# Performance work log

Hardware: AMD Instinct MI355X
Metric: run time of the kernel (lower is better)

The kernel has to match this reference:

```python
import jax, jax.numpy as jnp
import numpy as np

B, L, D, H, DFF = 2, 2048, 1024, 16, 4096
DH = D // H  # 64
EPS = 1e-6


def setup_inputs() -> dict:
    key = jax.random.key(0)
    ks = jax.random.split(key, 12)
    s = 0.02  # weight init scale
    inp = {
        "x": jax.random.normal(ks[0], (B, L, D), jnp.float32),
        "Wq": jax.random.normal(ks[1], (D, D), jnp.float32) * s,
        "bq": jnp.zeros((D,), jnp.float32),
        "Wk": jax.random.normal(ks[2], (D, D), jnp.float32) * s,
        "bk": jnp.zeros((D,), jnp.float32),
        "Wv": jax.random.normal(ks[3], (D, D), jnp.float32) * s,
        "bv": jnp.zeros((D,), jnp.float32),
        "Wo": jax.random.normal(ks[4], (D, D), jnp.float32) * s,
        "bo": jnp.zeros((D,), jnp.float32),
        "E": jax.random.normal(ks[5], (L, DH), jnp.float32),  # max_seq==L rel. embeddings
        "W1": jax.random.normal(ks[6], (D, DFF), jnp.float32) * s,
        "b1": jnp.zeros((DFF,), jnp.float32),
        "W2": jax.random.normal(ks[7], (DFF, D), jnp.float32) * s,
        "b2": jnp.zeros((D,), jnp.float32),
        "g1": jnp.ones((D,), jnp.float32),
        "beta1": jnp.zeros((D,), jnp.float32),
        "g2": jnp.ones((D,), jnp.float32),
        "beta2": jnp.zeros((D,), jnp.float32),
    }
    return inp


def _layernorm(x, g, b):
    mu = jnp.mean(x, axis=-1, keepdims=True)
    var = jnp.mean(jnp.square(x - mu), axis=-1, keepdims=True)
    return (x - mu) * jax.lax.rsqrt(var + EPS) * g + b


def _qe_mask(qe):
    # keep entries where col j >= len_k - 1 - row i (upper-right triangle)
    lq, lk = qe.shape[-2], qe.shape[-1]
    keep = jnp.arange(lk)[None, :] >= (lk - 1 - jnp.arange(lq))[:, None]
    return qe * keep.astype(qe.dtype)


def _skew(qe):
    # Music-Transformer skewing: pad 1 on the left of last dim, reshape, drop first row
    b, h, lq, lk = qe.shape
    padded = jnp.pad(qe, ((0, 0), (0, 0), (0, 0), (1, 0)))  # [b,h,lq,lk+1]
    reshaped = padded.reshape(b, h, lk + 1, lq)
    return reshaped[:, :, 1:, :]  # [b,h,lk,lq] == [b,h,lq,lk] since lq==lk here


def reference(x, Wq, bq, Wk, bk, Wv, bv, Wo, bo, E, W1, b1, W2, b2, g1, beta1, g2, beta2):
    b, l, d = x.shape
    # projections -> [b, h, l, dh]
    def split_heads(t):
        return t.reshape(b, l, H, DH).transpose(0, 2, 1, 3)

    q = split_heads(x @ Wq + bq)
    k = split_heads(x @ Wk + bk)
    v = split_heads(x @ Wv + bv)

    # relative logits: E sliced to last len_q rows (len_q == max_seq here -> all of E)
    e = E[E.shape[0] - l:, :]  # [l, dh]
    qe = jnp.einsum("bhld,md->bhlm", q, e)
    srel = _skew(_qe_mask(qe))  # [b,h,l,l]

    logits = (jnp.einsum("bhld,bhmd->bhlm", q, k) + srel) / np.sqrt(DH).astype(np.float32)
    attn = jax.nn.softmax(logits, axis=-1)
    out = jnp.einsum("bhlm,bhmd->bhld", attn, v)
    out = out.transpose(0, 2, 1, 3).reshape(b, l, d)
    attn_out = out @ Wo + bo

    out1 = _layernorm(attn_out + x, g1, beta1)
    ffn = jax.nn.relu(out1 @ W1 + b1) @ W2 + b2
    out2 = _layernorm(out1 + ffn, g2, beta2)
    return out2
```

## Files before the change

kernel.cpp:

```cpp
#include <hip/hip_runtime.h>

typedef unsigned short u16;
typedef __attribute__((ext_vector_type(4))) short s16x4;
typedef __attribute__((ext_vector_type(8))) short s16x8;
typedef __attribute__((ext_vector_type(4))) float f32x4;

#define MFMA16(a,b,c) __builtin_amdgcn_mfma_f32_16x16x32_bf16((a),(b),(c),0,0,0)
#define LSEQ 2048
#define QSCALE 0.18033688011112042f

__device__ __forceinline__ u16 f2b(float f) {
  union { float f; unsigned u; } v; v.f = f;
  unsigned r = v.u + 0x7FFFu + ((v.u >> 16) & 1u);
  return (u16)(r >> 16);
}
__device__ __forceinline__ void g2l16(const void* g, void* l) {
  __builtin_amdgcn_global_load_lds(
      (const __attribute__((address_space(1))) unsigned int*)g,
      (__attribute__((address_space(3))) unsigned int*)l, 16, 0, 0);
}

__global__ __launch_bounds__(256) void k_prep_all(
    const float* __restrict__ x, const float* __restrict__ E,
    const float* __restrict__ bq, const float* __restrict__ bk, const float* __restrict__ bv,
    const float* __restrict__ Wq, const float* __restrict__ Wk, const float* __restrict__ Wv,
    const float* __restrict__ Wo, const float* __restrict__ W1, const float* __restrict__ W2,
    u16* __restrict__ xb, u16* __restrict__ Ebf, float* __restrict__ bcat,
    u16* __restrict__ Wqt, u16* __restrict__ Wot, u16* __restrict__ W1t, u16* __restrict__ W2t) {
  __shared__ float T[64][65];
  const int b = blockIdx.x, tid = threadIdx.x;

  if (b < 1056) {
    const float* src = (b < 1024) ? x : E;
    u16* dst = (b < 1024) ? xb : Ebf;
    const int base = (b < 1024) ? b * 4096 : (b - 1024) * 4096;
#pragma unroll
    for (int p = 0; p < 4; p++) {
      int i = base + p * 1024 + tid * 4;
      float4 v = *(const float4*)(src + i);
      ushort4 o;
      o.x = f2b(v.x); o.y = f2b(v.y); o.z = f2b(v.z); o.w = f2b(v.w);
      *(ushort4*)(dst + i) = o;
    }
    return;
  }
  if (b == 1056) {
    for (int i = tid; i < 3072; i += 256)
      bcat[i] = (i < 1024) ? bq[i] : (i < 2048) ? bk[i - 1024] : bv[i - 2048];
    return;
  }

  const int idx = b - 1057;
  const float* W; u16* Wt; int K, N, bx, by;
  if (idx < 1024) {
    const int m = idx >> 8, ti = idx & 255;
    const float* ws4[4] = {Wq, Wk, Wv, Wo};
    W = ws4[m];
    Wt = (m < 3) ? (Wqt + (size_t)m * 1048576) : Wot;
    K = 1024; N = 1024; bx = ti & 15; by = ti >> 4;
  } else if (idx < 2048) {
    const int ti = idx - 1024;
    W = W1; Wt = W1t; K = 1024; N = 4096; bx = ti & 63; by = ti >> 6;
  } else {
    const int ti = idx - 2048;
    W = W2; Wt = W2t; K = 4096; N = 1024; bx = ti & 15; by = ti >> 4;
  }
  const int k0 = by * 64, n0 = bx * 64;
  const int r = tid >> 4, c4 = (tid & 15) * 4;
#pragma unroll
  for (int i = 0; i < 4; i++) {
    float4 v = *(const float4*)(W + (size_t)(k0 + r + i * 16) * N + n0 + c4);
    T[r + i * 16][c4 + 0] = v.x; T[r + i * 16][c4 + 1] = v.y;
    T[r + i * 16][c4 + 2] = v.z; T[r + i * 16][c4 + 3] = v.w;
  }
  __syncthreads();
#pragma unroll
  for (int i = 0; i < 4; i++) {
    int nl = r + i * 16;
    ushort4 o;
    o.x = f2b(T[c4 + 0][nl]); o.y = f2b(T[c4 + 1][nl]);
    o.z = f2b(T[c4 + 2][nl]); o.w = f2b(T[c4 + 3][nl]);
    *(ushort4*)(Wt + (size_t)(n0 + nl) * K + k0 + c4) = o;
  }
}

template <int BN, int FLAGS>
__global__ __launch_bounds__(256) void k_gemm(const u16* __restrict__ A, const u16* __restrict__ Bt,
                                              const float* __restrict__ bias, const void* __restrict__ resid,
                                              void* __restrict__ Cout, int M, int N, int K) {
  constexpr int MI = (BN == 128) ? 4 : 2;
  __shared__ __align__(16) u16 As[2][128 * 32];
  __shared__ __align__(16) u16 Bs[2][BN * 32];
  const int tid = threadIdx.x;
  const int lane = tid & 63, wave = tid >> 6;
  const int lo = lane & 15, hi = lane >> 4;
  const int WROW = (BN == 128) ? (wave >> 1) * 64 : wave * 32;
  const int WCOL = (BN == 128) ? (wave & 1) * 64 : 0;
  const int m0 = blockIdx.y * 128, n0 = blockIdx.x * BN;

  const int colg = ((lane & 3) * 16) ^ (((lane >> 3) & 3) << 4);
  const int arow = wave * 32 + (lane >> 2);
  const int swzr = ((lane >> 1) & 3) << 4;

  f32x4 acc[MI][4];
#pragma unroll
  for (int mi = 0; mi < MI; mi++)
#pragma unroll
    for (int ni = 0; ni < 4; ni++) acc[mi][ni] = (f32x4){0.f, 0.f, 0.f, 0.f};

  const char* Ab = (const char*)A;
  const char* Bb = (const char*)Bt;
  const int nt = K >> 5;

  auto stage = [&](int buf, int t) {
    const int k0 = t * 32;
    char* ad = (char*)&As[buf][0] + wave * 2048;
    const char* as = Ab + ((size_t)(m0 + arow) * K + k0) * 2 + colg;
    g2l16(as, ad);
    g2l16(as + (size_t)16 * K * 2, ad + 1024);
    if (BN == 128) {
      char* bd = (char*)&Bs[buf][0] + wave * 2048;
      const char* bs = Bb + ((size_t)(n0 + arow) * K + k0) * 2 + colg;
      g2l16(bs, bd);
      g2l16(bs + (size_t)16 * K * 2, bd + 1024);
    } else {
      char* bd = (char*)&Bs[buf][0] + wave * 1024;
      const int brow = wave * 16 + (lane >> 2);
      const char* bs = Bb + ((size_t)(n0 + brow) * K + k0) * 2 + colg;
      g2l16(bs, bd);
    }
  };

  stage(0, 0);
  int buf = 0;
  for (int t = 0; t < nt; t++) {
    __syncthreads();
    if (t + 1 < nt) stage(buf ^ 1, t + 1);
    const char* ab = (const char*)&As[buf][0];
    const char* bb2 = (const char*)&Bs[buf][0];
    s16x8 af[MI], bfr[4];
#pragma unroll
    for (int mi = 0; mi < MI; mi++) {
      int row = WROW + mi * 16 + lo;
      af[mi] = *(const s16x8*)(ab + row * 64 + ((hi * 16) ^ swzr));
    }
#pragma unroll
    for (int ni = 0; ni < 4; ni++) {
      int row = WCOL + ni * 16 + lo;
      bfr[ni] = *(const s16x8*)(bb2 + row * 64 + ((hi * 16) ^ swzr));
    }
#pragma unroll
    for (int mi = 0; mi < MI; mi++)
#pragma unroll
      for (int ni = 0; ni < 4; ni++)
        acc[mi][ni] = MFMA16(af[mi], bfr[ni], acc[mi][ni]);
    buf ^= 1;
  }

#pragma unroll
  for (int mi = 0; mi < MI; mi++)
#pragma unroll
    for (int ni = 0; ni < 4; ni++) {
      const int mb = m0 + WROW + mi * 16 + hi * 4;
      const int n = n0 + WCOL + ni * 16 + lo;
      float v4[4];
#pragma unroll
      for (int reg = 0; reg < 4; reg++) {
        float v = acc[mi][ni][reg] + bias[n];
        if (FLAGS & 8) v += ((const float*)resid)[(size_t)(mb + reg) * N + n];
        if (FLAGS & 16) {
          union { unsigned u; float f; } q;
          q.u = ((unsigned)((const u16*)resid)[(size_t)(mb + reg) * N + n]) << 16;
          v += q.f;
        }
        if (FLAGS & 1) v = fmaxf(v, 0.f);
        v4[reg] = v;
      }
      if (FLAGS & 4) {
        const int seg = n >> 10, nn = n & 1023;
        const int hh = nn >> 6, dd = nn & 63;
        const int bb = mb >> 11, ll = mb & 2047;
        u16* dst = (u16*)Cout + (size_t)seg * 4194304;
        if (seg == 0) {
#pragma unroll
          for (int reg = 0; reg < 4; reg++)
            dst[((size_t)(bb * 16 + hh) * LSEQ + ll + reg) * 64 + dd] = f2b(v4[reg] * QSCALE);
        } else if (seg == 1) {
#pragma unroll
          for (int reg = 0; reg < 4; reg++)
            dst[((size_t)(bb * 16 + hh) * LSEQ + ll + reg) * 64 + dd] = f2b(v4[reg]);
        } else {
          ushort4 o;
          o.x = f2b(v4[0]); o.y = f2b(v4[1]); o.z = f2b(v4[2]); o.w = f2b(v4[3]);
          *(ushort4*)&((u16*)dst)[((size_t)(bb * 16 + hh) * 64 + dd) * LSEQ + ll] = o;
        }
      } else if (FLAGS & 2) {
        u16* dst = (u16*)Cout;
#pragma unroll
        for (int reg = 0; reg < 4; reg++) dst[(size_t)(mb + reg) * N + n] = f2b(v4[reg]);
      } else {
        float* dst = (float*)Cout;
#pragma unroll
        for (int reg = 0; reg < 4; reg++) dst[(size_t)(mb + reg) * N + n] = v4[reg];
      }
    }
}

__global__ __launch_bounds__(512, 4) void k_attn(const u16* __restrict__ Qh, const u16* __restrict__ Kh,
                                                 const u16* __restrict__ Vt, const u16* __restrict__ Eb,
                                                 u16* __restrict__ Ob) {
  __shared__ __align__(16) u16 Ksh[2][64 * 64];
  __shared__ __align__(16) u16 Vts[2][64 * 64];
  __shared__ __align__(16) float Gsh[8][16 * 84];

  const int tid = threadIdx.x;
  const int lane = tid & 63, wave = tid >> 6;
  const int lo = lane & 15, hi = lane >> 4;

  const int hb = blockIdx.x;
  const int x = hb & 7;
  const int kk = hb >> 3;
  const int bh = x * 4 + (kk >> 4);
  const int ti = (kk & 32) ? (15 - (kk & 15)) : (kk & 15);
  const int l0 = ti * 128;
  const int bb = bh >> 4, hh = bh & 15;
  const int lw = l0 + wave * 16;

  const u16* Qb = Qh + (size_t)bh * LSEQ * 64;
  const char* Kb = (const char*)(Kh + (size_t)bh * LSEQ * 64);
  const char* Vb = (const char*)(Vt + (size_t)bh * 64 * LSEQ);

  const int colsw = ((lane & 7) * 16) ^ (((lane >> 3) & 7) << 4);
  const int swzv = (lo & 7) << 4;
  const int c0 = (hi * 16) ^ swzv;

  auto stageKV = [&](int buf_, int j0_) {
    char* kd = (char*)&Ksh[buf_][0] + wave * 1024;
    const char* ks = Kb + (size_t)(j0_ + wave * 8 + (lane >> 3)) * 128 + colsw;
    g2l16(ks, kd);
    char* vd = (char*)&Vts[buf_][0] + wave * 1024;
    const char* vs = Vb + (size_t)(wave * 8 + (lane >> 3)) * (LSEQ * 2) + (size_t)j0_ * 2 + colsw;
    g2l16(vs, vd);
  };

  s16x8 aq[2];
  aq[0] = *(const s16x8*)(Qb + (size_t)(lw + lo) * 64 + hi * 8);
  aq[1] = *(const s16x8*)(Qb + (size_t)(lw + lo) * 64 + 32 + hi * 8);

  float m_run = -1e30f, l_run = 0.f;
  f32x4 oacc[4];
#pragma unroll
  for (int f = 0; f < 4; f++) oacc[f] = (f32x4){0.f, 0.f, 0.f, 0.f};

  float* gw = &Gsh[wave][0];

  stageKV(0, 0);
  int buf = 0;

  for (int t = 0; t < 32; t++) {
    const int j0 = t * 64;
    const bool has_rel = (j0 <= lw);
    __syncthreads();
    if (t < 31) stageKV(buf ^ 1, j0 + 64);

    f32x4 s4[4];
#pragma unroll
    for (int c = 0; c < 4; c++) {
      const char* krow = (const char*)&Ksh[buf][0] + (c * 16 + lo) * 128;
      s16x8 a0 = *(const s16x8*)(krow + c0);
      s16x8 a1 = *(const s16x8*)(krow + (c0 ^ 64));
      s4[c] = (f32x4){0.f, 0.f, 0.f, 0.f};
      s4[c] = MFMA16(a0, aq[0], s4[c]);
      s4[c] = MFMA16(a1, aq[1], s4[c]);
    }

    if (has_rel) {
      const int waveBase = 2032 - lw + j0;
      const u16* ep0 = Eb + (size_t)(waveBase + lo) * 64 + hi * 8;
      s16x8 ec0 = *(const s16x8*)(ep0);
      s16x8 ec1 = *(const s16x8*)(ep0 + 32);
#pragma unroll
      for (int c2 = 0; c2 < 5; c2++) {
        s16x8 en0, en1;
        if (c2 < 4) {
          const u16* epn = ep0 + (size_t)(c2 + 1) * 16 * 64;
          en0 = *(const s16x8*)(epn);
          en1 = *(const s16x8*)(epn + 32);
        }
        f32x4 g = (f32x4){0.f, 0.f, 0.f, 0.f};
        g = MFMA16(ec0, aq[0], g);
        g = MFMA16(ec1, aq[1], g);
        *(f32x4*)(gw + 84 * lo + c2 * 16 + 4 * hi) = g;
        if (c2 < 4) { ec0 = en0; ec1 = en1; }
      }
      const int dd = lw - j0;
      if (dd >= 64) {
#pragma unroll
        for (int c = 0; c < 4; c++)
#pragma unroll
          for (int reg = 0; reg < 4; reg++)
            s4[c][reg] += gw[83 * lo + 15 + c * 16 + 4 * hi + reg];
      } else {
        const int rmax = dd + lo;
#pragma unroll
        for (int c = 0; c < 4; c++)
#pragma unroll
          for (int reg = 0; reg < 4; reg++) {
            int jr = c * 16 + 4 * hi + reg;
            float g = gw[83 * lo + 15 + jr];
            s4[c][reg] += (jr <= rmax) ? g : 0.f;
          }
      }
    }

    s16x4 vA[4][2], vB2[4][2];
#pragma unroll
    for (int f = 0; f < 4; f++) {
      const char* vrow = (const char*)&Vts[buf][0] + (f * 16 + lo) * 128;
#pragma unroll
      for (int m = 0; m < 2; m++) {
        vA[f][m]  = *(const s16x4*)(vrow + ((64 * m + 8 * hi) ^ swzv));
        vB2[f][m] = *(const s16x4*)(vrow + ((64 * m + 8 * hi + 32) ^ swzv));
      }
    }

    float mta = fmaxf(fmaxf(fmaxf(s4[0][0], s4[0][1]), fmaxf(s4[0][2], s4[0][3])),
                      fmaxf(fmaxf(s4[1][0], s4[1][1]), fmaxf(s4[1][2], s4[1][3])));
    float mtb = fmaxf(fmaxf(fmaxf(s4[2][0], s4[2][1]), fmaxf(s4[2][2], s4[2][3])),
                      fmaxf(fmaxf(s4[3][0], s4[3][1]), fmaxf(s4[3][2], s4[3][3])));
    float mt = fmaxf(mta, mtb);
    mt = fmaxf(mt, __shfl_xor(mt, 16, 64));
    mt = fmaxf(mt, __shfl_xor(mt, 32, 64));
    if (!__all(mt - m_run <= 8.f)) {
      float mnew = fmaxf(m_run, mt);
      float scl = exp2f(m_run - mnew);
      m_run = mnew;
      l_run *= scl;
#pragma unroll
      for (int f = 0; f < 4; f++)
#pragma unroll
        for (int reg = 0; reg < 4; reg++) oacc[f][reg] *= scl;
    }

    unsigned w8[8];
    float psum = 0.f;
#pragma unroll
    for (int c = 0; c < 4; c++) {
      float a0 = exp2f(s4[c][0] - m_run), a1 = exp2f(s4[c][1] - m_run);
      float a2 = exp2f(s4[c][2] - m_run), a3 = exp2f(s4[c][3] - m_run);
      psum += (a0 + a1) + (a2 + a3);
      asm("v_cvt_pk_bf16_f32 %0, %1, %2" : "=v"(w8[c * 2]) : "v"(a0), "v"(a1));
      asm("v_cvt_pk_bf16_f32 %0, %1, %2" : "=v"(w8[c * 2 + 1]) : "v"(a2), "v"(a3));
    }

    union UU { uint4 u; s16x8 v; };
    UU pb0, pb1;
    pb0.u = make_uint4(w8[0], w8[1], w8[2], w8[3]);
    pb1.u = make_uint4(w8[4], w8[5], w8[6], w8[7]);

#pragma unroll
    for (int f = 0; f < 4; f++) {
      s16x8 v0 = __builtin_shufflevector(vA[f][0], vB2[f][0], 0, 1, 2, 3, 4, 5, 6, 7);
      s16x8 v1 = __builtin_shufflevector(vA[f][1], vB2[f][1], 0, 1, 2, 3, 4, 5, 6, 7);
      oacc[f] = MFMA16(v0, pb0.v, oacc[f]);
      oacc[f] = MFMA16(v1, pb1.v, oacc[f]);
    }

    psum += __shfl_xor(psum, 16, 64);
    psum += __shfl_xor(psum, 32, 64);
    l_run += psum;

    buf ^= 1;
  }

  const float inv = 1.f / l_run;
  const size_t orow = (size_t)(bb * LSEQ + lw + lo) * 1024 + hh * 64;
#pragma unroll
  for (int f = 0; f < 4; f++) {
    ushort4 o;
    o.x = f2b(oacc[f][0] * inv); o.y = f2b(oacc[f][1] * inv);
    o.z = f2b(oacc[f][2] * inv); o.w = f2b(oacc[f][3] * inv);
    *(ushort4*)(Ob + orow + f * 16 + 4 * hi) = o;
  }
}

__global__ __launch_bounds__(256) void k_layernorm(const float* __restrict__ X, const float* __restrict__ gw,
                                                   const float* __restrict__ bw, float* __restrict__ outF,
                                                   u16* __restrict__ outB) {
  __shared__ float red[2][4];
  const int row = blockIdx.x, tid = threadIdx.x;
  const int lane = tid & 63, wave = tid >> 6;
  const float* x = X + (size_t)row * 1024;
  float4 v = *(const float4*)(x + tid * 4);
  float s = v.x + v.y + v.z + v.w;
  float s2 = v.x * v.x + v.y * v.y + v.z * v.z + v.w * v.w;
#pragma unroll
  for (int msk = 1; msk <= 32; msk <<= 1) {
    s += __shfl_xor(s, msk, 64);
    s2 += __shfl_xor(s2, msk, 64);
  }
  if (lane == 0) { red[0][wave] = s; red[1][wave] = s2; }
  __syncthreads();
  s = red[0][0] + red[0][1] + red[0][2] + red[0][3];
  s2 = red[1][0] + red[1][1] + red[1][2] + red[1][3];
  float mean = s * (1.f / 1024.f);
  float var = s2 * (1.f / 1024.f) - mean * mean;
  float rs = rsqrtf(var + 1e-6f);
  float4 g4 = *(const float4*)(gw + tid * 4);
  float4 b4 = *(const float4*)(bw + tid * 4);
  float4 o;
  o.x = (v.x - mean) * rs * g4.x + b4.x;
  o.y = (v.y - mean) * rs * g4.y + b4.y;
  o.z = (v.z - mean) * rs * g4.z + b4.z;
  o.w = (v.w - mean) * rs * g4.w + b4.w;
  if (outF) *(float4*)(outF + (size_t)row * 1024 + tid * 4) = o;
  if (outB) {
    ushort4 ob;
    ob.x = f2b(o.x); ob.y = f2b(o.y); ob.z = f2b(o.z); ob.w = f2b(o.w);
    *(ushort4*)(outB + (size_t)row * 1024 + tid * 4) = ob;
  }
}

extern "C" void kernel_launch(void* const* d_in, const int* in_sizes, int n_in,
                              void* d_out, int out_size, void* d_ws, size_t ws_size,
                              hipStream_t stream) {
  const float* x   = (const float*)d_in[0];
  const float* Wq  = (const float*)d_in[1];
  const float* bq  = (const float*)d_in[2];
  const float* Wk  = (const float*)d_in[3];
  const float* bk  = (const float*)d_in[4];
  const float* Wv  = (const float*)d_in[5];
  const float* bv  = (const float*)d_in[6];
  const float* Wo  = (const float*)d_in[7];
  const float* bo  = (const float*)d_in[8];
  const float* E   = (const float*)d_in[9];
  const float* W1  = (const float*)d_in[10];
  const float* b1  = (const float*)d_in[11];
  const float* W2  = (const float*)d_in[12];
  const float* b2  = (const float*)d_in[13];
  const float* g1  = (const float*)d_in[14];
  const float* be1 = (const float*)d_in[15];
  const float* g2  = (const float*)d_in[16];
  const float* be2 = (const float*)d_in[17];

  char* ws = (char*)d_ws;
  const size_t MB = 1ull << 20;
  u16* Wqt = (u16*)(ws + 0 * MB);
  u16* Wot = (u16*)(ws + 6 * MB);
  u16* W1t = (u16*)(ws + 8 * MB);
  u16* W2t = (u16*)(ws + 16 * MB);
  u16* Ebf = (u16*)(ws + 24 * MB);
  float* bcat = (float*)(ws + 24 * MB + 512 * 1024);
  u16* xb  = (u16*)(ws + 25 * MB);
  u16* qb  = (u16*)(ws + 33 * MB);
  u16* kb  = (u16*)(ws + 41 * MB);
  u16* vt  = (u16*)(ws + 49 * MB);
  u16* ao  = (u16*)(ws + 57 * MB);
  float* t1 = (float*)(ws + 65 * MB);
  u16* o1b  = (u16*)(ws + 25 * MB);
  u16* h1b  = (u16*)(ws + 49 * MB);
  float* outF = (float*)d_out;

  k_prep_all<<<4129, 256, 0, stream>>>(x, E, bq, bk, bv, Wq, Wk, Wv, Wo, W1, W2,
                                       xb, Ebf, bcat, Wqt, Wot, W1t, W2t);

  k_gemm<128, 4><<<dim3(24, 32), 256, 0, stream>>>(xb, Wqt, bcat, nullptr, qb, 4096, 3072, 1024);

  k_attn<<<dim3(512), 512, 0, stream>>>(qb, kb, vt, Ebf, ao);

  k_gemm<64, 8><<<dim3(16, 32), 256, 0, stream>>>(ao, Wot, bo, x, t1, 4096, 1024, 1024);

  k_layernorm<<<4096, 256, 0, stream>>>(t1, g1, be1, nullptr, o1b);

  k_gemm<128, 3><<<dim3(32, 32), 256, 0, stream>>>(o1b, W1t, b1, nullptr, h1b, 4096, 4096, 1024);

  k_gemm<64, 16><<<dim3(16, 32), 256, 0, stream>>>(h1b, W2t, b2, o1b, outF, 4096, 1024, 4096);

  k_layernorm<<<4096, 256, 0, stream>>>(outF, g2, be2, outF, nullptr);
}
```

Measured before the change: 344.7 us.

## Hoist E loads, compute row sums via MFMA, add setprio around MFMA blocks

Issues all relative-embedding global loads at the top of each tile so their latency overlaps the QK MFMAs. Moves the V LDS reads to just before the PV MFMAs. Replaces the scalar exp-sum and cross-lane shuffles with an MFMA against a vector of bf16 ones. The row sum is then taken from the already-rounded bf16 probabilities, which keeps numerator and denominator consistent but changes rounding slightly. It also raises wave priority around the MFMA bursts and uses more registers to hold the preloaded E fragments.

```diff
diff --git a/kernel.cpp b/kernel.cpp
--- a/kernel.cpp
+++ b/kernel.cpp
@@ -247,6 +247,8 @@
   aq[0] = *(const s16x8*)(Qb + (size_t)(lw + lo) * 64 + hi * 8);
   aq[1] = *(const s16x8*)(Qb + (size_t)(lw + lo) * 64 + 32 + hi * 8);
 
+  const s16x8 ones8 = {16256, 16256, 16256, 16256, 16256, 16256, 16256, 16256};
+
   float m_run = -1e30f, l_run = 0.f;
   f32x4 oacc[4];
 #pragma unroll
@@ -263,6 +265,19 @@
     __syncthreads();
     if (t < 31) stageKV(buf ^ 1, j0 + 64);
 
+    s16x8 e0[5], e1[5];
+    if (has_rel) {
+      const int waveBase = 2032 - lw + j0;
+      const u16* ep = Eb + (size_t)(waveBase + lo) * 64 + hi * 8;
+#pragma unroll
+      for (int c2 = 0; c2 < 5; c2++) {
+        e0[c2] = *(const s16x8*)(ep);
+        e1[c2] = *(const s16x8*)(ep + 32);
+        ep += 16 * 64;
+      }
+    }
+
+    __builtin_amdgcn_s_setprio(1);
     f32x4 s4[4];
 #pragma unroll
     for (int c = 0; c < 4; c++) {
@@ -275,24 +290,17 @@
     }
 
     if (has_rel) {
-      const int waveBase = 2032 - lw + j0;
-      const u16* ep0 = Eb + (size_t)(waveBase + lo) * 64 + hi * 8;
-      s16x8 ec0 = *(const s16x8*)(ep0);
-      s16x8 ec1 = *(const s16x8*)(ep0 + 32);
 #pragma unroll
       for (int c2 = 0; c2 < 5; c2++) {
-        s16x8 en0, en1;
-        if (c2 < 4) {
-          const u16* epn = ep0 + (size_t)(c2 + 1) * 16 * 64;
-          en0 = *(const s16x8*)(epn);
-          en1 = *(const s16x8*)(epn + 32);
-        }
         f32x4 g = (f32x4){0.f, 0.f, 0.f, 0.f};
-        g = MFMA16(ec0, aq[0], g);
-        g = MFMA16(ec1, aq[1], g);
+        g = MFMA16(e0[c2], aq[0], g);
+        g = MFMA16(e1[c2], aq[1], g);
         *(f32x4*)(gw + 84 * lo + c2 * 16 + 4 * hi) = g;
-        if (c2 < 4) { ec0 = en0; ec1 = en1; }
-      }
+      }
+    }
+    __builtin_amdgcn_s_setprio(0);
+
+    if (has_rel) {
       const int dd = lw - j0;
       if (dd >= 64) {
 #pragma unroll
@@ -310,17 +318,6 @@
             float g = gw[83 * lo + 15 + jr];
             s4[c][reg] += (jr <= rmax) ? g : 0.f;
           }
-      }
-    }
-
-    s16x4 vA[4][2], vB2[4][2];
-#pragma unroll
-    for (int f = 0; f < 4; f++) {
-      const char* vrow = (const char*)&Vts[buf][0] + (f * 16 + lo) * 128;
-#pragma unroll
-      for (int m = 0; m < 2; m++) {
-        vA[f][m]  = *(const s16x4*)(vrow + ((64 * m + 8 * hi) ^ swzv));
-        vB2[f][m] = *(const s16x4*)(vrow + ((64 * m + 8 * hi + 32) ^ swzv));
       }
     }
 
@@ -343,12 +340,10 @@
     }
 
     unsigned w8[8];
-    float psum = 0.f;
 #pragma unroll
     for (int c = 0; c < 4; c++) {
       float a0 = exp2f(s4[c][0] - m_run), a1 = exp2f(s4[c][1] - m_run);
       float a2 = exp2f(s4[c][2] - m_run), a3 = exp2f(s4[c][3] - m_run);
-      psum += (a0 + a1) + (a2 + a3);
       asm("v_cvt_pk_bf16_f32 %0, %1, %2" : "=v"(w8[c * 2]) : "v"(a0), "v"(a1));
       asm("v_cvt_pk_bf16_f32 %0, %1, %2" : "=v"(w8[c * 2 + 1]) : "v"(a2), "v"(a3));
     }
@@ -357,6 +352,22 @@
     UU pb0, pb1;
     pb0.u = make_uint4(w8[0], w8[1], w8[2], w8[3]);
     pb1.u = make_uint4(w8[4], w8[5], w8[6], w8[7]);
+
+    s16x4 vA[4][2], vB2[4][2];
+#pragma unroll
+    for (int f = 0; f < 4; f++) {
+      const char* vrow = (const char*)&Vts[buf][0] + (f * 16 + lo) * 128;
+#pragma unroll
+      for (int m = 0; m < 2; m++) {
+        vA[f][m]  = *(const s16x4*)(vrow + ((64 * m + 8 * hi) ^ swzv));
+        vB2[f][m] = *(const s16x4*)(vrow + ((64 * m + 8 * hi + 32) ^ swzv));
+      }
+    }
+
+    __builtin_amdgcn_s_setprio(1);
+    f32x4 ps = (f32x4){0.f, 0.f, 0.f, 0.f};
+    ps = MFMA16(ones8, pb0.v, ps);
+    ps = MFMA16(ones8, pb1.v, ps);
 
 #pragma unroll
     for (int f = 0; f < 4; f++) {
@@ -365,11 +376,9 @@
       oacc[f] = MFMA16(v0, pb0.v, oacc[f]);
       oacc[f] = MFMA16(v1, pb1.v, oacc[f]);
     }
-
-    psum += __shfl_xor(psum, 16, 64);
-    psum += __shfl_xor(psum, 32, 64);
-    l_run += psum;
-
+    __builtin_amdgcn_s_setprio(0);
+
+    l_run += ps[0];
     buf ^= 1;
   }
 
```

Measured after the change: 375.9 us. +9.1%, slower.

## Use 256-row GEMM tiles for wide GEMMs and MFMA row sums in attention

Applied to the files above, without the earlier changes.

Adds a BM template parameter to the GEMM. The QKV and FFN-up GEMMs now run with 256x128 tiles on 512-thread blocks, which halves the number of B-tile reloads per output and raises reuse. In attention, the per-lane softmax denominator is no longer built with scalar adds and cross-lane shuffles. It is computed by two extra MFMAs against a vector of bf16 ones, wrapped in s_setprio to favour the matrix work. The trade-offs are larger blocks with fewer blocks in the grid, higher register pressure under the new launch bounds, and a denominator summed from bf16-rounded probabilities.

```diff
diff --git a/kernel.cpp b/kernel.cpp
--- a/kernel.cpp
+++ b/kernel.cpp
@@ -84,19 +84,20 @@
   }
 }
 
-template <int BN, int FLAGS>
-__global__ __launch_bounds__(256) void k_gemm(const u16* __restrict__ A, const u16* __restrict__ Bt,
-                                              const float* __restrict__ bias, const void* __restrict__ resid,
-                                              void* __restrict__ Cout, int M, int N, int K) {
+template <int BM, int BN, int FLAGS>
+__global__ __launch_bounds__(BM == 256 ? 512 : 256, BM == 256 ? 4 : 2)
+void k_gemm(const u16* __restrict__ A, const u16* __restrict__ Bt,
+            const float* __restrict__ bias, const void* __restrict__ resid,
+            void* __restrict__ Cout, int M, int N, int K) {
   constexpr int MI = (BN == 128) ? 4 : 2;
-  __shared__ __align__(16) u16 As[2][128 * 32];
+  __shared__ __align__(16) u16 As[2][BM * 32];
   __shared__ __align__(16) u16 Bs[2][BN * 32];
   const int tid = threadIdx.x;
   const int lane = tid & 63, wave = tid >> 6;
   const int lo = lane & 15, hi = lane >> 4;
   const int WROW = (BN == 128) ? (wave >> 1) * 64 : wave * 32;
   const int WCOL = (BN == 128) ? (wave & 1) * 64 : 0;
-  const int m0 = blockIdx.y * 128, n0 = blockIdx.x * BN;
+  const int m0 = blockIdx.y * BM, n0 = blockIdx.x * BN;
 
   const int colg = ((lane & 3) * 16) ^ (((lane >> 3) & 3) << 4);
   const int arow = wave * 32 + (lane >> 2);
@@ -118,7 +119,11 @@
     const char* as = Ab + ((size_t)(m0 + arow) * K + k0) * 2 + colg;
     g2l16(as, ad);
     g2l16(as + (size_t)16 * K * 2, ad + 1024);
-    if (BN == 128) {
+    if (BM == 256) {
+      char* bd = (char*)&Bs[buf][0] + wave * 1024;
+      const char* bs = Bb + ((size_t)(n0 + wave * 16 + (lane >> 2)) * K + k0) * 2 + colg;
+      g2l16(bs, bd);
+    } else if (BN == 128) {
       char* bd = (char*)&Bs[buf][0] + wave * 2048;
       const char* bs = Bb + ((size_t)(n0 + arow) * K + k0) * 2 + colg;
       g2l16(bs, bd);
@@ -247,6 +252,8 @@
   aq[0] = *(const s16x8*)(Qb + (size_t)(lw + lo) * 64 + hi * 8);
   aq[1] = *(const s16x8*)(Qb + (size_t)(lw + lo) * 64 + 32 + hi * 8);
 
+  const s16x8 ones8 = {16256, 16256, 16256, 16256, 16256, 16256, 16256, 16256};
+
   float m_run = -1e30f, l_run = 0.f;
   f32x4 oacc[4];
 #pragma unroll
@@ -343,12 +350,10 @@
     }
 
     unsigned w8[8];
-    float psum = 0.f;
 #pragma unroll
     for (int c = 0; c < 4; c++) {
       float a0 = exp2f(s4[c][0] - m_run), a1 = exp2f(s4[c][1] - m_run);
       float a2 = exp2f(s4[c][2] - m_run), a3 = exp2f(s4[c][3] - m_run);
-      psum += (a0 + a1) + (a2 + a3);
       asm("v_cvt_pk_bf16_f32 %0, %1, %2" : "=v"(w8[c * 2]) : "v"(a0), "v"(a1));
       asm("v_cvt_pk_bf16_f32 %0, %1, %2" : "=v"(w8[c * 2 + 1]) : "v"(a2), "v"(a3));
     }
@@ -357,6 +362,11 @@
     UU pb0, pb1;
     pb0.u = make_uint4(w8[0], w8[1], w8[2], w8[3]);
     pb1.u = make_uint4(w8[4], w8[5], w8[6], w8[7]);
+
+    __builtin_amdgcn_s_setprio(1);
+    f32x4 ps = (f32x4){0.f, 0.f, 0.f, 0.f};
+    ps = MFMA16(ones8, pb0.v, ps);
+    ps = MFMA16(ones8, pb1.v, ps);
 
 #pragma unroll
     for (int f = 0; f < 4; f++) {
@@ -365,11 +375,9 @@
       oacc[f] = MFMA16(v0, pb0.v, oacc[f]);
       oacc[f] = MFMA16(v1, pb1.v, oacc[f]);
     }
-
-    psum += __shfl_xor(psum, 16, 64);
-    psum += __shfl_xor(psum, 32, 64);
-    l_run += psum;
-
+    __builtin_amdgcn_s_setprio(0);
+
+    l_run += ps[0];
     buf ^= 1;
   }
 
@@ -464,17 +472,17 @@
   k_prep_all<<<4129, 256, 0, stream>>>(x, E, bq, bk, bv, Wq, Wk, Wv, Wo, W1, W2,
                                        xb, Ebf, bcat, Wqt, Wot, W1t, W2t);
 
-  k_gemm<128, 4><<<dim3(24, 32), 256, 0, stream>>>(xb, Wqt, bcat, nullptr, qb, 4096, 3072, 1024);
+  k_gemm<256, 128, 4><<<dim3(24, 16), 512, 0, stream>>>(xb, Wqt, bcat, nullptr, qb, 4096, 3072, 1024);
 
   k_attn<<<dim3(512), 512, 0, stream>>>(qb, kb, vt, Ebf, ao);
 
-  k_gemm<64, 8><<<dim3(16, 32), 256, 0, stream>>>(ao, Wot, bo, x, t1, 4096, 1024, 1024);
+  k_gemm<128, 64, 8><<<dim3(16, 32), 256, 0, stream>>>(ao, Wot, bo, x, t1, 4096, 1024, 1024);
 
   k_layernorm<<<4096, 256, 0, stream>>>(t1, g1, be1, nullptr, o1b);
 
-  k_gemm<128, 3><<<dim3(32, 32), 256, 0, stream>>>(o1b, W1t, b1, nullptr, h1b, 4096, 4096, 1024);
-
-  k_gemm<64, 16><<<dim3(16, 32), 256, 0, stream>>>(h1b, W2t, b2, o1b, outF, 4096, 1024, 4096);
+  k_gemm<256, 128, 3><<<dim3(32, 16), 512, 0, stream>>>(o1b, W1t, b1, nullptr, h1b, 4096, 4096, 1024);
+
+  k_gemm<128, 64, 16><<<dim3(16, 32), 256, 0, stream>>>(h1b, W2t, b2, o1b, outF, 4096, 1024, 4096);
 
   k_layernorm<<<4096, 256, 0, stream>>>(outF, g2, be2, outF, nullptr);
 }
```

Result: no change. 339.6 us (-1.5%).
